# Kernel tuning notes

Hardware: AMD Instinct MI355X
Metric: run time of the kernel (lower is better)

Reference implementation:

```python
import jax, jax.numpy as jnp
import numpy as np

B, N, C, H = 2, 2048, 1024, 16
HD = C // H  # head dim = 64


def setup_inputs() -> dict:
    key = jax.random.key(0)
    kq, kk, kv, km = jax.random.split(key, 4)
    q = jax.random.normal(kq, (B, N, C), dtype=jnp.float32)
    k = jax.random.normal(kk, (B, N, C), dtype=jnp.float32)
    v = jax.random.normal(kv, (B, N, C), dtype=jnp.float32)
    mask = jax.random.randint(km, (B, 1, N, N), 0, 2, dtype=jnp.int32)
    return {"q": q, "k": k, "v": v, "mask": mask}


def reference(q, k, v, mask):
    b, n, c = q.shape
    # (B, N, C) -> (B, H, N, HD)
    qh = q.reshape(b, n, H, HD).transpose(0, 2, 1, 3)
    kh = k.reshape(b, n, H, HD).transpose(0, 2, 1, 3)
    vh = v.reshape(b, n, H, HD).transpose(0, 2, 1, 3)
    scale = 1.0 / jnp.sqrt(jnp.float32(HD))
    # scores: (B, H, N, N)
    scores = jnp.einsum("bhqd,bhkd->bhqk", qh, kh) * scale
    scores = jnp.where(mask == 0, jnp.float32(-1e9), scores)
    probs = jax.nn.softmax(scores, axis=-1)
    atten = jnp.einsum("bhqk,bhkd->bhqd", probs, vh)
    # (B, H, N, HD) -> (B, N, C)
    return atten.transpose(0, 2, 1, 3).reshape(b, n, c)
```

## Files before the change

### kernel.cpp

```cpp
#include <hip/hip_runtime.h>
#include <hip/hip_bf16.h>

#define B_ 2
#define N_ 2048
#define C_ 1024
#define H_ 16
#define HD_ 64

#define KT 64
#define NT (N_ / KT)
#define TILE_E 4096
#define PSTR 72
#define NW 8
#define QB 128

#define NWM 4
#define QBM 64

typedef short s16x8 __attribute__((ext_vector_type(8)));
typedef short s16x4 __attribute__((ext_vector_type(4)));
typedef float f32x4 __attribute__((ext_vector_type(4)));

__device__ __forceinline__ s16x8 cvt8(float4 a, float4 b) {
    union { s16x8 v; __hip_bfloat162 h[4]; } u;
    u.h[0] = __float22bfloat162_rn(float2{a.x, a.y});
    u.h[1] = __float22bfloat162_rn(float2{a.z, a.w});
    u.h[2] = __float22bfloat162_rn(float2{b.x, b.y});
    u.h[3] = __float22bfloat162_rn(float2{b.z, b.w});
    return u.v;
}

__device__ __forceinline__ void gll16(const void* g, void* l) {
    __builtin_amdgcn_global_load_lds(
        (const __attribute__((address_space(1))) unsigned*)g,
        (__attribute__((address_space(3))) unsigned*)l, 16, 0, 0);
}

__global__ __launch_bounds__(256)
void pack_mask(const int* __restrict__ M, unsigned long long* __restrict__ bits) {
    const int gw   = (blockIdx.x * 256 + threadIdx.x) >> 6;
    const int lane = threadIdx.x & 63;
#pragma unroll
    for (int it = 0; it < 16; ++it) {
        const size_t wi = (size_t)gw * 16 + it;
        unsigned long long bal = __ballot(M[wi * 64 + lane] != 0);
        if (lane == 0) bits[wi] = bal;
    }
}

__global__ __launch_bounds__(256)
void prepass(const int* __restrict__ M, const float* __restrict__ K,
             const float* __restrict__ V, unsigned long long* __restrict__ bits,
             ushort* __restrict__ Kw, ushort* __restrict__ Vw) {
    const int bid = blockIdx.x;
    const int tid = threadIdx.x;
    if (bid < 2048) {
        const int gt = bid * 256 + tid;
        const int4* src = (const int4*)M + (size_t)gt * 4;
        unsigned r = 0;
#pragma unroll
        for (int c = 0; c < 4; ++c) {
            const int4 m4 = src[c];
            r |= (m4.x != 0 ? 1u : 0u) << (c * 4 + 0);
            r |= (m4.y != 0 ? 1u : 0u) << (c * 4 + 1);
            r |= (m4.z != 0 ? 1u : 0u) << (c * 4 + 2);
            r |= (m4.w != 0 ? 1u : 0u) << (c * 4 + 3);
        }
        ((ushort*)bits)[gt] = (ushort)r;
    } else if (bid < 4096) {
        const int gt = (bid - 2048) * 256 + tid;
        const int b  = gt >> 18;
        const int h  = (gt >> 14) & 15;
        const int n  = (gt >> 3) & 2047;
        const int db = gt & 7;
        const size_t src = (size_t)(b * N_ + n) * C_ + h * 64 + db * 8;
        float4 f0 = *(const float4*)(K + src);
        float4 f1 = *(const float4*)(K + src + 4);
        const int key = n & 63, kt = n >> 6;
        const int p = (key & 32) | ((key & 4) << 2) | ((key >> 1) & 12) | (key & 3);
        ushort* dst = Kw + (size_t)((b * H_ + h) * NT + kt) * TILE_E
                         + p * 64 + ((db ^ (p & 7)) * 8);
        *(s16x8*)dst = cvt8(f0, f1);
    } else {
        const int gt  = (bid - 4096) * 256 + tid;
        const int b   = gt >> 16;
        const int h   = (gt >> 12) & 15;
        const int kt  = (gt >> 7) & 31;
        const int kb4 = (gt >> 3) & 15;
        const int db  = gt & 7;
        const int key0 = kb4 * 4;
        float f[4][8];
#pragma unroll
        for (int i = 0; i < 4; ++i) {
            const size_t src = (size_t)(b * N_ + kt * 64 + key0 + i) * C_ + h * 64 + db * 8;
            *(float4*)&f[i][0] = *(const float4*)(V + src);
            *(float4*)&f[i][4] = *(const float4*)(V + src + 4);
        }
        ushort* tb = Vw + (size_t)((b * H_ + h) * NT + kt) * TILE_E;
#pragma unroll
        for (int j = 0; j < 8; ++j) {
            const int d = db * 8 + j;
            union { s16x4 v; __hip_bfloat162 h2[2]; } u;
            u.h2[0] = __float22bfloat162_rn(float2{f[0][j], f[1][j]});
            u.h2[1] = __float22bfloat162_rn(float2{f[2][j], f[3][j]});
            *(s16x4*)(tb + d * 64 + (((key0 >> 3) ^ (d & 7)) * 8) + (key0 & 7)) = u.v;
        }
    }
}

__global__ __launch_bounds__(256, 4)
void mha_fwd(const float* __restrict__ Q, const ushort* __restrict__ Kw,
             const ushort* __restrict__ Vw, const unsigned* __restrict__ bits,
             float* __restrict__ O) {
    __shared__ ushort Kl[2][TILE_E];
    __shared__ ushort Vt[2][TILE_E];

    const int sid = blockIdx.x;
    const int jj  = sid >> 3;
    const int hb  = ((sid & 7) << 2) | (jj & 3);
    const int qt  = jj >> 2;
    const int h   = hb & 15;
    const int b   = hb >> 4;

    const int tid  = threadIdx.x;
    const int w    = tid >> 6;
    const int lane = tid & 63;
    const int l16  = lane & 15;
    const int quad = lane >> 4;

    const size_t head_off = (size_t)b * N_ * C_ + (size_t)h * HD_;
    const int qb = qt * QBM + w * 16;

    const float qs = 0.125f * 1.44269504088896f;
    const size_t qoff = head_off + (size_t)(qb + l16) * C_ + quad * 8;
    float4 q0 = *(const float4*)(Q + qoff);
    float4 q1 = *(const float4*)(Q + qoff + 4);
    float4 q2 = *(const float4*)(Q + qoff + 32);
    float4 q3 = *(const float4*)(Q + qoff + 36);
    q0.x*=qs; q0.y*=qs; q0.z*=qs; q0.w*=qs;
    q1.x*=qs; q1.y*=qs; q1.z*=qs; q1.w*=qs;
    q2.x*=qs; q2.y*=qs; q2.z*=qs; q2.w*=qs;
    q3.x*=qs; q3.y*=qs; q3.z*=qs; q3.w*=qs;
    const s16x8 qa0 = cvt8(q0, q1);
    const s16x8 qa1 = cvt8(q2, q3);

    s16x8 onesb;
#pragma unroll
    for (int i = 0; i < 8; ++i) onesb[i] = (short)0x3F80;

    f32x4 acc[4];
#pragma unroll
    for (int c = 0; c < 4; ++c) acc[c] = f32x4{0.f, 0.f, 0.f, 0.f};
    f32x4 sum = f32x4{0.f, 0.f, 0.f, 0.f};

    const int fbase = l16 * 64 + ((quad ^ (l16 & 7)) * 8);

    const size_t tilebase = (size_t)((b * H_ + h) * NT) * TILE_E;
    const ushort* Kg = Kw + tilebase + (size_t)tid * 8;
    const ushort* Vg = Vw + tilebase + (size_t)tid * 8;

    const unsigned* mq = bits + ((size_t)b * N_ + qb + l16) * (N_ / 32);

    gll16(Kg,        &Kl[0][w * 512]);
    gll16(Kg + 2048, &Kl[0][w * 512 + 2048]);
    gll16(Vg,        &Vt[0][w * 512]);
    gll16(Vg + 2048, &Vt[0][w * 512 + 2048]);
    const ushort* Kg_pf = Kg + TILE_E;
    const ushort* Vg_pf = Vg + TILE_E;

    uint4 mw = *(const uint4*)mq;  mq += 4;

    for (int kt2 = 0; kt2 < NT; kt2 += 2) {
        const uint4 mw_nxt = *(const uint4*)mq;  mq += 4;
        const bool pf1 = (kt2 + 2 < NT);
#pragma unroll
        for (int u = 0; u < 2; ++u) {
            __syncthreads();
            if (u == 0 || pf1) {
                gll16(Kg_pf,        &Kl[1 - u][w * 512]);
                gll16(Kg_pf + 2048, &Kl[1 - u][w * 512 + 2048]);
                gll16(Vg_pf,        &Vt[1 - u][w * 512]);
                gll16(Vg_pf + 2048, &Vt[1 - u][w * 512 + 2048]);
                Kg_pf += TILE_E;  Vg_pf += TILE_E;
            }
            const unsigned w0 = u ? mw.z : mw.x;
            const unsigned w1 = u ? mw.w : mw.y;

            f32x4 s[4];
            __builtin_amdgcn_s_setprio(1);
#pragma unroll
            for (int t = 0; t < 4; ++t) {
                s16x8 kb0 = *(const s16x8*)(&Kl[u][fbase + t * 1024]);
                s16x8 kb1 = *(const s16x8*)(&Kl[u][(fbase ^ 32) + t * 1024]);
                f32x4 z = {0.f, 0.f, 0.f, 0.f};
                z = __builtin_amdgcn_mfma_f32_16x16x32_bf16(kb0, qa0, z, 0, 0, 0);
                z = __builtin_amdgcn_mfma_f32_16x16x32_bf16(kb1, qa1, z, 0, 0, 0);
                s[t] = z;
            }
            __builtin_amdgcn_s_setprio(0);

            const unsigned aw0 = w0 >> (quad * 8);
            const unsigned aw1 = w1 >> (quad * 8);
            union { s16x8 v; __hip_bfloat162 h2[4]; } pk0, pk1;
#pragma unroll
            for (int t = 0; t < 4; ++t) {
                const unsigned aw = ((t < 2) ? aw0 : aw1) >> ((t & 1) * 4);
                float p0 = __builtin_amdgcn_exp2f(((aw >> 0) & 1u) ? s[t][0] : -1e9f);
                float p1 = __builtin_amdgcn_exp2f(((aw >> 1) & 1u) ? s[t][1] : -1e9f);
                float p2 = __builtin_amdgcn_exp2f(((aw >> 2) & 1u) ? s[t][2] : -1e9f);
                float p3 = __builtin_amdgcn_exp2f(((aw >> 3) & 1u) ? s[t][3] : -1e9f);
                __hip_bfloat162 lo = __float22bfloat162_rn(float2{p0, p1});
                __hip_bfloat162 hi = __float22bfloat162_rn(float2{p2, p3});
                if      (t == 0) { pk0.h2[0] = lo; pk0.h2[1] = hi; }
                else if (t == 1) { pk0.h2[2] = lo; pk0.h2[3] = hi; }
                else if (t == 2) { pk1.h2[0] = lo; pk1.h2[1] = hi; }
                else             { pk1.h2[2] = lo; pk1.h2[3] = hi; }
            }

            __builtin_amdgcn_s_setprio(1);
#pragma unroll
            for (int half = 0; half < 2; ++half) {
                const s16x8 pa = half ? pk1.v : pk0.v;
#pragma unroll
                for (int c = 0; c < 4; ++c) {
                    const int vidx = (half ? (fbase ^ 32) : fbase) + c * 1024;
                    s16x8 vb = *(const s16x8*)(&Vt[u][vidx]);
                    acc[c] = __builtin_amdgcn_mfma_f32_16x16x32_bf16(pa, vb, acc[c], 0, 0, 0);
                }
                sum = __builtin_amdgcn_mfma_f32_16x16x32_bf16(pa, onesb, sum, 0, 0, 0);
            }
            __builtin_amdgcn_s_setprio(0);
        }
        mw = mw_nxt;
    }

#pragma unroll
    for (int r = 0; r < 4; ++r) {
        const float inv = 1.0f / sum[r];
        const size_t obase = head_off + (size_t)(qb + quad * 4 + r) * C_;
        O[obase + l16]      = acc[0][r] * inv;
        O[obase + l16 + 16] = acc[1][r] * inv;
        O[obase + l16 + 32] = acc[2][r] * inv;
        O[obase + l16 + 48] = acc[3][r] * inv;
    }
}

#define KSTR 72
#define VSTR 72
__global__ __launch_bounds__(512, 4)
void mha_fwd_fb(const float* __restrict__ Q, const float* __restrict__ K,
                const float* __restrict__ V, const unsigned* __restrict__ bits,
                float* __restrict__ O) {
    __shared__ ushort Kl[2][KT * KSTR];
    __shared__ ushort Vt[2][HD_ * VSTR];
    __shared__ ushort Pl[NW][16 * PSTR];
    const int qt = blockIdx.x, h = blockIdx.y, b = blockIdx.z, tid = threadIdx.x;
    const int w = tid >> 6, lane = tid & 63, l16 = lane & 15, quad = lane >> 4;
    const size_t head_off = (size_t)b * N_ * C_ + (size_t)h * HD_;
    const int qb = qt * QB + w * 16;
    const float qs = 0.125f * 1.44269504088896f;
    const size_t qoff = head_off + (size_t)(qb + l16) * C_ + quad * 8;
    float4 q0 = *(const float4*)(Q + qoff);
    float4 q1 = *(const float4*)(Q + qoff + 4);
    float4 q2 = *(const float4*)(Q + qoff + 32);
    float4 q3 = *(const float4*)(Q + qoff + 36);
    q0.x*=qs; q0.y*=qs; q0.z*=qs; q0.w*=qs;
    q1.x*=qs; q1.y*=qs; q1.z*=qs; q1.w*=qs;
    q2.x*=qs; q2.y*=qs; q2.z*=qs; q2.w*=qs;
    q3.x*=qs; q3.y*=qs; q3.z*=qs; q3.w*=qs;
    const s16x8 qa0 = cvt8(q0, q1);
    const s16x8 qa1 = cvt8(q2, q3);
    f32x4 acc[4];
#pragma unroll
    for (int c = 0; c < 4; ++c) acc[c] = f32x4{0.f, 0.f, 0.f, 0.f};
    float lsum = 0.f;
    const int skey = tid >> 3, sd0 = (tid & 7) * 8;
    const int kp = tid >> 4, vd0 = (tid & 15) * 4;
    const int vcol = 2 * (kp & 3) + ((((kp >> 2) ^ (vd0 >> 3)) & 7) << 3);
    const unsigned* brow = bits + ((size_t)b * N_ + qb + l16) * (N_ / 32);
    const float SHIFT = 16.0f;
    {
        const size_t kbase = head_off + (size_t)skey * C_ + sd0;
        float4 kA = *(const float4*)(K + kbase);
        float4 kB = *(const float4*)(K + kbase + 4);
        *(s16x8*)(&Kl[0][skey * KSTR + sd0]) = cvt8(kA, kB);
        const size_t vbase = head_off + (size_t)(2 * kp) * C_ + vd0;
        float4 vA = *(const float4*)(V + vbase);
        float4 vB = *(const float4*)(V + vbase + C_);
        const float* ap = (const float*)&vA;
        const float* bp = (const float*)&vB;
#pragma unroll
        for (int i = 0; i < 4; ++i) {
            __hip_bfloat162 pr = __float22bfloat162_rn(float2{ap[i], bp[i]});
            *(unsigned*)(&Vt[0][(vd0 + i) * VSTR + vcol]) = *(unsigned*)&pr;
        }
    }
    for (int kt = 0; kt < NT; ++kt) {
        const int cur = kt & 1;
        float4 kA, kB, vA, vB;
        const bool has_next = (kt + 1 < NT);
        if (has_next) {
            const size_t kbase = head_off + (size_t)((kt + 1) * KT + skey) * C_ + sd0;
            kA = *(const float4*)(K + kbase);
            kB = *(const float4*)(K + kbase + 4);
            const size_t vbase = head_off + (size_t)((kt + 1) * KT + 2 * kp) * C_ + vd0;
            vA = *(const float4*)(V + vbase);
            vB = *(const float4*)(V + vbase + C_);
        }
        const unsigned w0 = brow[2 * kt];
        const unsigned w1 = brow[2 * kt + 1];
        __syncthreads();
        f32x4 s[4];
#pragma unroll
        for (int t = 0; t < 4; ++t) {
            s16x8 kb0 = *(const s16x8*)(&Kl[cur][(t * 16 + l16) * KSTR + quad * 8]);
            s16x8 kb1 = *(const s16x8*)(&Kl[cur][(t * 16 + l16) * KSTR + quad * 8 + 32]);
            f32x4 z = {0.f, 0.f, 0.f, 0.f};
            z = __builtin_amdgcn_mfma_f32_16x16x32_bf16(kb0, qa0, z, 0, 0, 0);
            z = __builtin_amdgcn_mfma_f32_16x16x32_bf16(kb1, qa1, z, 0, 0, 0);
            s[t] = z;
        }
        const unsigned a0 = w0 >> (quad * 4);
        const unsigned a1 = w1 >> (quad * 4);
#pragma unroll
        for (int t = 0; t < 4; ++t) {
            const unsigned aw = (t < 2) ? a0 : a1;
            const int sh = (t & 1) * 16;
            float p0 = exp2f((((aw >> (sh + 0)) & 1u) ? s[t][0] : -1e9f) - SHIFT);
            float p1 = exp2f((((aw >> (sh + 1)) & 1u) ? s[t][1] : -1e9f) - SHIFT);
            float p2 = exp2f((((aw >> (sh + 2)) & 1u) ? s[t][2] : -1e9f) - SHIFT);
            float p3 = exp2f((((aw >> (sh + 3)) & 1u) ? s[t][3] : -1e9f) - SHIFT);
            lsum += (p0 + p1) + (p2 + p3);
            union { s16x4 v; __hip_bfloat162 h2[2]; } uu;
            uu.h2[0] = __float22bfloat162_rn(float2{p0, p1});
            uu.h2[1] = __float22bfloat162_rn(float2{p2, p3});
            *(s16x4*)(&Pl[w][l16 * PSTR + t * 16 + quad * 4]) = uu.v;
        }
#pragma unroll
        for (int half = 0; half < 2; ++half) {
            s16x8 pa = *(const s16x8*)(&Pl[w][l16 * PSTR + half * 32 + quad * 8]);
#pragma unroll
            for (int c = 0; c < 4; ++c) {
                const int dr = c * 16 + l16;
                const int blk = (half * 4 + quad) ^ ((dr >> 3) & 7);
                s16x8 vb = *(const s16x8*)(&Vt[cur][dr * VSTR + blk * 8]);
                acc[c] = __builtin_amdgcn_mfma_f32_16x16x32_bf16(pa, vb, acc[c], 0, 0, 0);
            }
        }
        if (has_next) {
            *(s16x8*)(&Kl[1 - cur][skey * KSTR + sd0]) = cvt8(kA, kB);
            const float* ap = (const float*)&vA;
            const float* bp = (const float*)&vB;
#pragma unroll
            for (int i = 0; i < 4; ++i) {
                __hip_bfloat162 pr = __float22bfloat162_rn(float2{ap[i], bp[i]});
                *(unsigned*)(&Vt[1 - cur][(vd0 + i) * VSTR + vcol]) = *(unsigned*)&pr;
            }
        }
    }
    lsum += __shfl_xor(lsum, 16);
    lsum += __shfl_xor(lsum, 32);
#pragma unroll
    for (int r = 0; r < 4; ++r) {
        const float inv = 1.0f / __shfl(lsum, quad * 4 + r);
        const size_t obase = head_off + (size_t)(qb + quad * 4 + r) * C_;
        O[obase + l16]      = acc[0][r] * inv;
        O[obase + l16 + 16] = acc[1][r] * inv;
        O[obase + l16 + 32] = acc[2][r] * inv;
        O[obase + l16 + 48] = acc[3][r] * inv;
    }
}

extern "C" void kernel_launch(void* const* d_in, const int* in_sizes, int n_in,
                              void* d_out, int out_size, void* d_ws, size_t ws_size,
                              hipStream_t stream) {
    const float* q = (const float*)d_in[0];
    const float* k = (const float*)d_in[1];
    const float* v = (const float*)d_in[2];
    const int*   m = (const int*)d_in[3];
    float*       o = (float*)d_out;

    const size_t BITS_BYTES = (size_t)B_ * N_ * N_ / 8;
    const size_t KV_BYTES   = (size_t)B_ * H_ * N_ * HD_ * 2;
    const size_t NEED       = BITS_BYTES + 2 * KV_BYTES;

    unsigned long long* bits = (unsigned long long*)d_ws;

    if (ws_size >= NEED) {
        ushort* kw = (ushort*)((char*)d_ws + BITS_BYTES);
        ushort* vw = (ushort*)((char*)d_ws + BITS_BYTES + KV_BYTES);
        hipLaunchKernelGGL(prepass, dim3(4608), dim3(256), 0, stream,
                           m, k, v, bits, kw, vw);
        hipLaunchKernelGGL(mha_fwd, dim3(1024), dim3(256), 0, stream,
                           q, kw, vw, (const unsigned*)bits, o);
    } else {
        hipLaunchKernelGGL(pack_mask, dim3(2048), dim3(256), 0, stream, m, bits);
        dim3 grid(N_ / QB, H_, B_);
        hipLaunchKernelGGL(mha_fwd_fb, grid, dim3(512), 0, stream,
                           q, k, v, (const unsigned*)bits, o);
    }
}
```

Baseline: 165.7 us.

## Switch attention kernel to 32x32x16 MFMA with 32 query rows per wave

Replaces the 16x16x32 bf16 MFMA tiles with 32x32x16 MFMA. Each wave now handles 32 query rows and each block 128 rows, so the grid is halved and every K/V tile staged in LDS is reused across twice as many queries. The K prepass permutation, the LDS fragment addressing, the mask bit extraction and the output layout are all rewritten to match the new accumulator layout. In exchange, register pressure rises and the occupancy hint is dropped from launch bounds, which may lower occupancy and leaves fewer blocks (512) to spread across the CUs.

```diff
diff --git a/kernel.cpp b/kernel.cpp
--- a/kernel.cpp
+++ b/kernel.cpp
@@ -14,12 +14,12 @@
 #define NW 8
 #define QB 128
 
-#define NWM 4
-#define QBM 64
+#define QBM 128
 
 typedef short s16x8 __attribute__((ext_vector_type(8)));
 typedef short s16x4 __attribute__((ext_vector_type(4)));
 typedef float f32x4 __attribute__((ext_vector_type(4)));
+typedef float f32x16 __attribute__((ext_vector_type(16)));
 
 __device__ __forceinline__ s16x8 cvt8(float4 a, float4 b) {
     union { s16x8 v; __hip_bfloat162 h[4]; } u;
@@ -77,7 +77,8 @@
         float4 f0 = *(const float4*)(K + src);
         float4 f1 = *(const float4*)(K + src + 4);
         const int key = n & 63, kt = n >> 6;
-        const int p = (key & 32) | ((key & 4) << 2) | ((key >> 1) & 12) | (key & 3);
+        const int p = (key & 32) | ((key & 4) << 2) | ((key & 16) >> 1)
+                    | ((key & 8) >> 1) | (key & 3);
         ushort* dst = Kw + (size_t)((b * H_ + h) * NT + kt) * TILE_E
                          + p * 64 + ((db ^ (p & 7)) * 8);
         *(s16x8*)dst = cvt8(f0, f1);
@@ -108,7 +109,7 @@
     }
 }
 
-__global__ __launch_bounds__(256, 4)
+__global__ __launch_bounds__(256)
 void mha_fwd(const float* __restrict__ Q, const ushort* __restrict__ Kw,
              const ushort* __restrict__ Vw, const unsigned* __restrict__ bits,
              float* __restrict__ O) {
@@ -125,41 +126,38 @@
     const int tid  = threadIdx.x;
     const int w    = tid >> 6;
     const int lane = tid & 63;
-    const int l16  = lane & 15;
-    const int quad = lane >> 4;
+    const int rl   = lane & 31;
+    const int hh   = lane >> 5;
+    const int e3   = rl & 7;
 
     const size_t head_off = (size_t)b * N_ * C_ + (size_t)h * HD_;
-    const int qb = qt * QBM + w * 16;
+    const int qb = qt * QBM + w * 32;
 
     const float qs = 0.125f * 1.44269504088896f;
-    const size_t qoff = head_off + (size_t)(qb + l16) * C_ + quad * 8;
-    float4 q0 = *(const float4*)(Q + qoff);
-    float4 q1 = *(const float4*)(Q + qoff + 4);
-    float4 q2 = *(const float4*)(Q + qoff + 32);
-    float4 q3 = *(const float4*)(Q + qoff + 36);
-    q0.x*=qs; q0.y*=qs; q0.z*=qs; q0.w*=qs;
-    q1.x*=qs; q1.y*=qs; q1.z*=qs; q1.w*=qs;
-    q2.x*=qs; q2.y*=qs; q2.z*=qs; q2.w*=qs;
-    q3.x*=qs; q3.y*=qs; q3.z*=qs; q3.w*=qs;
-    const s16x8 qa0 = cvt8(q0, q1);
-    const s16x8 qa1 = cvt8(q2, q3);
+    const size_t qoff = head_off + (size_t)(qb + rl) * C_ + hh * 8;
+    s16x8 qa[4];
+#pragma unroll
+    for (int i = 0; i < 4; ++i) {
+        float4 a = *(const float4*)(Q + qoff + i * 16);
+        float4 c = *(const float4*)(Q + qoff + i * 16 + 4);
+        a.x*=qs; a.y*=qs; a.z*=qs; a.w*=qs;
+        c.x*=qs; c.y*=qs; c.z*=qs; c.w*=qs;
+        qa[i] = cvt8(a, c);
+    }
 
     s16x8 onesb;
 #pragma unroll
     for (int i = 0; i < 8; ++i) onesb[i] = (short)0x3F80;
 
-    f32x4 acc[4];
-#pragma unroll
-    for (int c = 0; c < 4; ++c) acc[c] = f32x4{0.f, 0.f, 0.f, 0.f};
-    f32x4 sum = f32x4{0.f, 0.f, 0.f, 0.f};
-
-    const int fbase = l16 * 64 + ((quad ^ (l16 & 7)) * 8);
+    f32x16 acc0, acc1, sum;
+#pragma unroll
+    for (int j = 0; j < 16; ++j) { acc0[j] = 0.f; acc1[j] = 0.f; sum[j] = 0.f; }
 
     const size_t tilebase = (size_t)((b * H_ + h) * NT) * TILE_E;
     const ushort* Kg = Kw + tilebase + (size_t)tid * 8;
     const ushort* Vg = Vw + tilebase + (size_t)tid * 8;
 
-    const unsigned* mq = bits + ((size_t)b * N_ + qb + l16) * (N_ / 32);
+    const unsigned* mq = bits + ((size_t)b * N_ + qb + rl) * (N_ / 32);
 
     gll16(Kg,        &Kl[0][w * 512]);
     gll16(Kg + 2048, &Kl[0][w * 512 + 2048]);
@@ -171,8 +169,10 @@
     uint4 mw = *(const uint4*)mq;  mq += 4;
 
     for (int kt2 = 0; kt2 < NT; kt2 += 2) {
-        const uint4 mw_nxt = *(const uint4*)mq;  mq += 4;
         const bool pf1 = (kt2 + 2 < NT);
+        uint4 mw_nxt = mw;
+        if (pf1) { mw_nxt = *(const uint4*)mq; }
+        mq += 4;
 #pragma unroll
         for (int u = 0; u < 2; ++u) {
             __syncthreads();
@@ -183,51 +183,57 @@
                 gll16(Vg_pf + 2048, &Vt[1 - u][w * 512 + 2048]);
                 Kg_pf += TILE_E;  Vg_pf += TILE_E;
             }
-            const unsigned w0 = u ? mw.z : mw.x;
-            const unsigned w1 = u ? mw.w : mw.y;
-
-            f32x4 s[4];
+
+            f32x16 z0, z1;
+#pragma unroll
+            for (int j = 0; j < 16; ++j) { z0[j] = 0.f; z1[j] = 0.f; }
             __builtin_amdgcn_s_setprio(1);
 #pragma unroll
-            for (int t = 0; t < 4; ++t) {
-                s16x8 kb0 = *(const s16x8*)(&Kl[u][fbase + t * 1024]);
-                s16x8 kb1 = *(const s16x8*)(&Kl[u][(fbase ^ 32) + t * 1024]);
-                f32x4 z = {0.f, 0.f, 0.f, 0.f};
-                z = __builtin_amdgcn_mfma_f32_16x16x32_bf16(kb0, qa0, z, 0, 0, 0);
-                z = __builtin_amdgcn_mfma_f32_16x16x32_bf16(kb1, qa1, z, 0, 0, 0);
-                s[t] = z;
+            for (int i = 0; i < 4; ++i) {
+                const int cb = ((i << 1) | hh) ^ e3;
+                s16x8 k0 = *(const s16x8*)(&Kl[u][rl * 64 + (cb << 3)]);
+                s16x8 k1 = *(const s16x8*)(&Kl[u][(rl + 32) * 64 + (cb << 3)]);
+                z0 = __builtin_amdgcn_mfma_f32_32x32x16_bf16(k0, qa[i], z0, 0, 0, 0);
+                z1 = __builtin_amdgcn_mfma_f32_32x32x16_bf16(k1, qa[i], z1, 0, 0, 0);
             }
             __builtin_amdgcn_s_setprio(0);
 
-            const unsigned aw0 = w0 >> (quad * 8);
-            const unsigned aw1 = w1 >> (quad * 8);
-            union { s16x8 v; __hip_bfloat162 h2[4]; } pk0, pk1;
-#pragma unroll
-            for (int t = 0; t < 4; ++t) {
-                const unsigned aw = ((t < 2) ? aw0 : aw1) >> ((t & 1) * 4);
-                float p0 = __builtin_amdgcn_exp2f(((aw >> 0) & 1u) ? s[t][0] : -1e9f);
-                float p1 = __builtin_amdgcn_exp2f(((aw >> 1) & 1u) ? s[t][1] : -1e9f);
-                float p2 = __builtin_amdgcn_exp2f(((aw >> 2) & 1u) ? s[t][2] : -1e9f);
-                float p3 = __builtin_amdgcn_exp2f(((aw >> 3) & 1u) ? s[t][3] : -1e9f);
-                __hip_bfloat162 lo = __float22bfloat162_rn(float2{p0, p1});
-                __hip_bfloat162 hi = __float22bfloat162_rn(float2{p2, p3});
-                if      (t == 0) { pk0.h2[0] = lo; pk0.h2[1] = hi; }
-                else if (t == 1) { pk0.h2[2] = lo; pk0.h2[3] = hi; }
-                else if (t == 2) { pk1.h2[0] = lo; pk1.h2[1] = hi; }
-                else             { pk1.h2[2] = lo; pk1.h2[3] = hi; }
-            }
+            const unsigned g0 = (u ? mw.z : mw.x) >> (hh * 8);
+            const unsigned g1 = (u ? mw.w : mw.y) >> (hh * 8);
+            s16x8 pa[4];
+            auto soft = [&](const f32x16& z, unsigned wg, s16x8& fA, s16x8& fB) {
+                float p[16];
+#pragma unroll
+                for (int R = 0; R < 4; ++R) {
+                    const int base = ((R & 1) << 4) + ((R >> 1) << 2);
+#pragma unroll
+                    for (int r = 0; r < 4; ++r)
+                        p[4 * R + r] = __builtin_amdgcn_exp2f(
+                            ((wg >> (base + r)) & 1u) ? z[4 * R + r] : -1e9f);
+                }
+                union { s16x8 v; __hip_bfloat162 h2[4]; } uA, uB;
+                uA.h2[0] = __float22bfloat162_rn(float2{p[0], p[1]});
+                uA.h2[1] = __float22bfloat162_rn(float2{p[2], p[3]});
+                uA.h2[2] = __float22bfloat162_rn(float2{p[8], p[9]});
+                uA.h2[3] = __float22bfloat162_rn(float2{p[10], p[11]});
+                uB.h2[0] = __float22bfloat162_rn(float2{p[4], p[5]});
+                uB.h2[1] = __float22bfloat162_rn(float2{p[6], p[7]});
+                uB.h2[2] = __float22bfloat162_rn(float2{p[12], p[13]});
+                uB.h2[3] = __float22bfloat162_rn(float2{p[14], p[15]});
+                fA = uA.v;  fB = uB.v;
+            };
+            soft(z0, g0, pa[0], pa[1]);
+            soft(z1, g1, pa[2], pa[3]);
 
             __builtin_amdgcn_s_setprio(1);
 #pragma unroll
-            for (int half = 0; half < 2; ++half) {
-                const s16x8 pa = half ? pk1.v : pk0.v;
-#pragma unroll
-                for (int c = 0; c < 4; ++c) {
-                    const int vidx = (half ? (fbase ^ 32) : fbase) + c * 1024;
-                    s16x8 vb = *(const s16x8*)(&Vt[u][vidx]);
-                    acc[c] = __builtin_amdgcn_mfma_f32_16x16x32_bf16(pa, vb, acc[c], 0, 0, 0);
-                }
-                sum = __builtin_amdgcn_mfma_f32_16x16x32_bf16(pa, onesb, sum, 0, 0, 0);
+            for (int i = 0; i < 4; ++i) {
+                const int cb = ((i << 1) | hh) ^ e3;
+                s16x8 v0 = *(const s16x8*)(&Vt[u][rl * 64 + (cb << 3)]);
+                s16x8 v1 = *(const s16x8*)(&Vt[u][(rl + 32) * 64 + (cb << 3)]);
+                acc0 = __builtin_amdgcn_mfma_f32_32x32x16_bf16(pa[i], v0, acc0, 0, 0, 0);
+                acc1 = __builtin_amdgcn_mfma_f32_32x32x16_bf16(pa[i], v1, acc1, 0, 0, 0);
+                sum  = __builtin_amdgcn_mfma_f32_32x32x16_bf16(pa[i], onesb, sum, 0, 0, 0);
             }
             __builtin_amdgcn_s_setprio(0);
         }
@@ -235,13 +241,12 @@
     }
 
 #pragma unroll
-    for (int r = 0; r < 4; ++r) {
-        const float inv = 1.0f / sum[r];
-        const size_t obase = head_off + (size_t)(qb + quad * 4 + r) * C_;
-        O[obase + l16]      = acc[0][r] * inv;
-        O[obase + l16 + 16] = acc[1][r] * inv;
-        O[obase + l16 + 32] = acc[2][r] * inv;
-        O[obase + l16 + 48] = acc[3][r] * inv;
+    for (int reg = 0; reg < 16; ++reg) {
+        const int qrow = qb + (reg & 3) + ((reg >> 2) << 3) + (hh << 2);
+        const float inv = 1.0f / sum[reg];
+        const size_t ob = head_off + (size_t)qrow * C_;
+        O[ob + rl]      = acc0[reg] * inv;
+        O[ob + rl + 32] = acc1[reg] * inv;
     }
 }
 
@@ -391,7 +396,7 @@
         ushort* vw = (ushort*)((char*)d_ws + BITS_BYTES + KV_BYTES);
         hipLaunchKernelGGL(prepass, dim3(4608), dim3(256), 0, stream,
                            m, k, v, bits, kw, vw);
-        hipLaunchKernelGGL(mha_fwd, dim3(1024), dim3(256), 0, stream,
+        hipLaunchKernelGGL(mha_fwd, dim3(512), dim3(256), 0, stream,
                            q, kw, vw, (const unsigned*)bits, o);
     } else {
         hipLaunchKernelGGL(pack_mask, dim3(2048), dim3(256), 0, stream, m, bits);
```

Result: no change. 167.5 us (+1.1%).
